# Kernel tuning notes

Measured on AMD Instinct MI355X. Metric: run time of the kernel, lower is better.

The kernel has to match this reference:

```python
import jax, jax.numpy as jnp
import numpy as np

# dims matching init_kwargs
B, C, T = 64, 8, 2048
K, DIL = 16, 4            # kernel_size, dilation
MLP = 16                  # mlp_dim
NF = min(MLP, K // 2 + 1) # n_frequencies = 9
FEAT = C * NF * 2         # 144
H1, H2 = 64, 32           # ReLUBlock hidden dims (64 -> 64//2)
EFF = DIL * (K - 1)       # 60
W = T - EFF               # 1988 windows


def setup_inputs() -> dict:
    key = jax.random.key(0)
    ks = jax.random.split(key, 10)
    def lin(k, out_d, in_d):
        kw, kb = jax.random.split(k)
        bound = 1.0 / np.sqrt(in_d)
        w = jax.random.uniform(kw, (out_d, in_d), jnp.float32, -bound, bound)
        b = jax.random.uniform(kb, (out_d,), jnp.float32, -bound, bound)
        return w, b
    x = jax.random.normal(ks[0], (B, C, T), jnp.float32)
    proj_w, proj_b = lin(ks[1], MLP, FEAT)
    w1, b1 = lin(ks[2], H1, MLP)
    w2, b2 = lin(ks[3], H2, H1)
    out_w, out_b = lin(ks[4], 1, H2)
    agg_w = jax.random.normal(ks[5], (W,), jnp.float32) * 0.1
    return {"x": x, "proj_w": proj_w, "proj_b": proj_b, "w1": w1, "b1": b1,
            "w2": w2, "b2": b2, "out_w": out_w, "out_b": out_b, "agg_w": agg_w}


def reference(x, proj_w, proj_b, w1, b1, w2, b2, out_w, out_b, agg_w):
    # Build all dilated windows at once: window[t, j] = x[..., t - (K-1-j)*DIL]
    starts = jnp.arange(EFF, T)                      # [W]
    offs = -(K - 1 - jnp.arange(K)) * DIL            # [K]
    idx = starts[:, None] + offs[None, :]            # [W, K]
    win = x[:, :, idx]                               # [B, C, W, K]
    f = jnp.fft.rfft(win, axis=-1)[..., :NF]         # [B, C, W, NF]
    mag = jnp.log1p(jnp.abs(f))
    ph = jnp.angle(f) / jnp.pi
    feat = jnp.stack([mag, ph], axis=-1)             # [B, C, W, NF, 2]
    feat = feat.transpose(0, 2, 1, 3, 4).reshape(B, W, FEAT)  # [B, W, C*NF*2]
    p = jnp.tanh(feat @ proj_w.T + proj_b) * jnp.pi  # [B, W, MLP]
    h = jax.nn.relu(p @ w1.T + b1)                   # [B, W, H1]
    h = jax.nn.relu(h @ w2.T + b2)                   # [B, W, H2]
    out = (h @ out_w.T + out_b)[..., 0]              # [B, W]
    wts = jax.nn.softmax(agg_w)                      # [W]
    return (out * wts[None, :]).sum(axis=1)          # [B]
```

## Files before the change

### kernel.cpp

```cpp
#include <hip/hip_runtime.h>
#include <math.h>

#define B_    64
#define C_    8
#define T_    2048
#define K_    16
#define NF_   9
#define FEAT_ 144
#define MLP_  16
#define H1_   64
#define H2_   32
#define EFF_  60
#define W_    1988
#define NWCH_ 8
#define NG_   4
#define PI_F  3.14159265358979323846f

constexpr float COS16[16] = {
   1.0f,  0.92387953251128674f,  0.70710678118654752f,  0.38268343236508977f,
   0.0f, -0.38268343236508977f, -0.70710678118654752f, -0.92387953251128674f,
  -1.0f, -0.92387953251128674f, -0.70710678118654752f, -0.38268343236508977f,
   0.0f,  0.38268343236508977f,  0.70710678118654752f,  0.92387953251128674f };
constexpr float SIN16F[16] = {
   0.0f,  0.38268343236508977f,  0.70710678118654752f,  0.92387953251128674f,
   1.0f,  0.92387953251128674f,  0.70710678118654752f,  0.38268343236508977f,
   0.0f, -0.38268343236508977f, -0.70710678118654752f, -0.92387953251128674f,
  -1.0f, -0.92387953251128674f, -0.70710678118654752f, -0.38268343236508977f };

__device__ __forceinline__ float fast_log1p(float s) {
  return __builtin_amdgcn_logf(1.0f + s) * 0.69314718055994531f;
}

__device__ __forceinline__ float atanpi_poly(float r) {
  const float s2 = r * r;
  float p = -0.0037310f;
  p = fmaf(p, s2,  0.0167600f);
  p = fmaf(p, s2, -0.0370617f);
  p = fmaf(p, s2,  0.0616068f);
  p = fmaf(p, s2, -0.10587734f);
  p = fmaf(p, s2,  0.31830265f);
  return r * p;
}

__device__ __forceinline__ float atan2pi_fast(float im, float re) {
  const float ax = fabsf(re), ay = fabsf(im);
  const float mx = fmaxf(ax, ay), mn = fminf(ax, ay);
  const float r = mn * __builtin_amdgcn_rcpf(fmaxf(mx, 1e-37f));
  float t = atanpi_poly(r);
  t = (ay > ax) ? 0.5f - t : t;
  t = (__float_as_uint(re) & 0x80000000u) ? 1.0f - t : t;
  return copysignf(t, im);
}

__device__ __forceinline__ float fast_tanh(float z) {
  const float az = fabsf(z);
  const float e = __builtin_amdgcn_exp2f(-2.8853900817779268f * az);
  const float th = fmaf(-2.0f, e * __builtin_amdgcn_rcpf(1.0f + e), 1.0f);
  return copysignf(th, z);
}

__device__ __forceinline__ void dft_proj_channel(const float* __restrict__ xc,
                                                 const float* __restrict__ PWt,
                                                 int c, float* pacc) {
  float win[K_];
  #pragma unroll
  for (int k = 0; k < K_; k++) win[k] = xc[k * 4];
  float ae[8], bo[8];
  #pragma unroll
  for (int k = 0; k < 8; k++) { ae[k] = win[k] + win[k+8]; bo[k] = win[k] - win[k+8]; }
  #pragma unroll
  for (int n = 0; n < NF_; n++) {
    float re = 0.f, im = 0.f;
    #pragma unroll
    for (int k = 0; k < 8; k++) {
      const float v = (n & 1) ? bo[k] : ae[k];
      const int t = (n * k) & 15;
      re = fmaf(v,  COS16[t],  re);
      im = fmaf(v, -SIN16F[t], im);
    }
    const float s   = __builtin_amdgcn_sqrtf(fmaf(re, re, im * im));
    const float mag = fast_log1p(s);
    const float ph  = atan2pi_fast(im, re);
    const float* rm = PWt + (size_t)((c * NF_ + n) * 2) * MLP_;
    #pragma unroll
    for (int j = 0; j < MLP_; j++)
      pacc[j] = fmaf(mag, rm[j], fmaf(ph, rm[MLP_ + j], pacc[j]));
  }
}

__device__ __forceinline__ float mlp_tail(const float* p,
                                          const float* __restrict__ w1, const float* __restrict__ b1,
                                          const float* __restrict__ W2t, const float* __restrict__ b2,
                                          const float* __restrict__ out_w, const float* __restrict__ out_b) {
  float h2a[H2_];
  #pragma unroll
  for (int m = 0; m < H2_; m++) h2a[m] = b2[m];
  #pragma unroll 8
  for (int i = 0; i < H1_; i++) {
    const float* r1 = w1 + i * MLP_;
    float acc = b1[i];
    #pragma unroll
    for (int j = 0; j < MLP_; j++) acc = fmaf(p[j], r1[j], acc);
    const float h1v = fmaxf(acc, 0.f);
    const float* r2 = W2t + i * H2_;
    #pragma unroll
    for (int m = 0; m < H2_; m++) h2a[m] = fmaf(h1v, r2[m], h2a[m]);
  }
  float o = out_b[0];
  #pragma unroll
  for (int m = 0; m < H2_; m++) o = fmaf(fmaxf(h2a[m], 0.f), out_w[m], o);
  return o;
}

__global__ __launch_bounds__(256) void setup_kernel(const float* __restrict__ agg,
                                                    float* __restrict__ wts,
                                                    const float* __restrict__ pw,
                                                    const float* __restrict__ w2,
                                                    float* __restrict__ PWt,
                                                    float* __restrict__ W2t) {
  if (blockIdx.x == 0) {
    __shared__ float red[256];
    const int tid = threadIdx.x;
    float m = -INFINITY;
    for (int i = tid; i < W_; i += 256) m = fmaxf(m, agg[i]);
    red[tid] = m; __syncthreads();
    for (int s = 128; s > 0; s >>= 1) { if (tid < s) red[tid] = fmaxf(red[tid], red[tid+s]); __syncthreads(); }
    const float mx = red[0];
    __syncthreads();
    float sum = 0.f;
    for (int i = tid; i < W_; i += 256) sum += expf(agg[i] - mx);
    red[tid] = sum; __syncthreads();
    for (int s = 128; s > 0; s >>= 1) { if (tid < s) red[tid] += red[tid+s]; __syncthreads(); }
    const float inv = 1.f / red[0];
    for (int i = tid; i < W_; i += 256) wts[i] = expf(agg[i] - mx) * inv;
  } else {
    const int tid = (blockIdx.x - 1) * 256 + threadIdx.x;
    if (tid < MLP_ * FEAT_) {
      const int j = tid / FEAT_, f = tid - j * FEAT_;
      PWt[f * MLP_ + j] = pw[tid];
    }
    if (tid < H2_ * H1_) {
      const int m = tid >> 6, i = tid & 63;
      W2t[i * H2_ + m] = w2[tid];
    }
  }
}

__global__ __launch_bounds__(256) void tcn_stage1(const float* __restrict__ x,
                                                  const float* __restrict__ PWt,
                                                  float* __restrict__ pf) {
  const int tid = threadIdx.x;
  const int b = blockIdx.y, g = blockIdx.z;
  const int w = blockIdx.x * 256 + tid;
  if (w >= W_) return;
  float pacc[MLP_];
  #pragma unroll
  for (int j = 0; j < MLP_; j++) pacc[j] = 0.f;
  #pragma unroll 1
  for (int cc = 0; cc < 2; cc++) {
    const int c = g * 2 + cc;
    dft_proj_channel(x + ((size_t)b * C_ + c) * T_ + w, PWt, c, pacc);
  }
  float4* dst = reinterpret_cast<float4*>(pf + ((size_t)(b * NG_ + g) * W_ + w) * MLP_);
  #pragma unroll
  for (int q = 0; q < 4; q++)
    dst[q] = make_float4(pacc[4*q+0], pacc[4*q+1], pacc[4*q+2], pacc[4*q+3]);
}

__global__ __launch_bounds__(256) void tcn_stage2(const float* __restrict__ pf,
                                                  const float* __restrict__ proj_b,
                                                  const float* __restrict__ w1, const float* __restrict__ b1,
                                                  const float* __restrict__ W2t, const float* __restrict__ b2,
                                                  const float* __restrict__ out_w, const float* __restrict__ out_b,
                                                  const float* __restrict__ wts, float* __restrict__ partials) {
  __shared__ float red[256];
  const int tid = threadIdx.x;
  const int b = blockIdx.y;
  const int w = blockIdx.x * 256 + tid;
  float val = 0.f;
  if (w < W_) {
    float pacc[MLP_];
    #pragma unroll
    for (int j = 0; j < MLP_; j++) pacc[j] = proj_b[j];
    #pragma unroll
    for (int g = 0; g < NG_; g++) {
      const float4* src = reinterpret_cast<const float4*>(pf + ((size_t)(b * NG_ + g) * W_ + w) * MLP_);
      #pragma unroll
      for (int q = 0; q < 4; q++) {
        const float4 a = src[q];
        pacc[4*q+0] += a.x; pacc[4*q+1] += a.y; pacc[4*q+2] += a.z; pacc[4*q+3] += a.w;
      }
    }
    float p[MLP_];
    #pragma unroll
    for (int j = 0; j < MLP_; j++) p[j] = fast_tanh(pacc[j]) * PI_F;
    val = mlp_tail(p, w1, b1, W2t, b2, out_w, out_b) * wts[w];
  }
  red[tid] = val; __syncthreads();
  for (int s = 128; s > 0; s >>= 1) { if (tid < s) red[tid] += red[tid+s]; __syncthreads(); }
  if (tid == 0) partials[b * NWCH_ + blockIdx.x] = red[0];
}

__global__ __launch_bounds__(256) void tcn_mono(const float* __restrict__ x,
                                                const float* __restrict__ PWt, const float* __restrict__ proj_b,
                                                const float* __restrict__ w1, const float* __restrict__ b1,
                                                const float* __restrict__ W2t, const float* __restrict__ b2,
                                                const float* __restrict__ out_w, const float* __restrict__ out_b,
                                                const float* __restrict__ wts, float* __restrict__ partials) {
  __shared__ float red[256];
  const int tid = threadIdx.x;
  const int b = blockIdx.y;
  const int w = blockIdx.x * 256 + tid;
  float val = 0.f;
  if (w < W_) {
    float pacc[MLP_];
    #pragma unroll
    for (int j = 0; j < MLP_; j++) pacc[j] = proj_b[j];
    #pragma unroll 1
    for (int c = 0; c < C_; c++)
      dft_proj_channel(x + ((size_t)b * C_ + c) * T_ + w, PWt, c, pacc);
    float p[MLP_];
    #pragma unroll
    for (int j = 0; j < MLP_; j++) p[j] = fast_tanh(pacc[j]) * PI_F;
    val = mlp_tail(p, w1, b1, W2t, b2, out_w, out_b) * wts[w];
  }
  red[tid] = val; __syncthreads();
  for (int s = 128; s > 0; s >>= 1) { if (tid < s) red[tid] += red[tid+s]; __syncthreads(); }
  if (tid == 0) partials[b * NWCH_ + blockIdx.x] = red[0];
}

__global__ void finalize_kernel(const float* __restrict__ partials, float* __restrict__ out) {
  const int b = threadIdx.x;
  if (b < B_) {
    float s = 0.f;
    #pragma unroll
    for (int c = 0; c < NWCH_; c++) s += partials[b * NWCH_ + c];
    out[b] = s;
  }
}

extern "C" void kernel_launch(void* const* d_in, const int* in_sizes, int n_in,
                              void* d_out, int out_size, void* d_ws, size_t ws_size,
                              hipStream_t stream) {
  const float* x      = (const float*)d_in[0];
  const float* proj_w = (const float*)d_in[1];
  const float* proj_b = (const float*)d_in[2];
  const float* w1     = (const float*)d_in[3];
  const float* b1     = (const float*)d_in[4];
  const float* w2     = (const float*)d_in[5];
  const float* b2     = (const float*)d_in[6];
  const float* out_w  = (const float*)d_in[7];
  const float* out_b  = (const float*)d_in[8];
  const float* agg_w  = (const float*)d_in[9];

  float* wts      = (float*)d_ws;
  float* partials = (float*)d_ws + 2048;
  float* PWt      = (float*)d_ws + 4096;
  float* W2t      = (float*)d_ws + 4096 + 2304;
  float* pf       = (float*)d_ws + 16384;

  const size_t need = ((size_t)16384 + (size_t)B_ * NG_ * W_ * MLP_) * sizeof(float);

  setup_kernel<<<10, 256, 0, stream>>>(agg_w, wts, proj_w, w2, PWt, W2t);
  if (ws_size >= need) {
    tcn_stage1<<<dim3(NWCH_, B_, NG_), 256, 0, stream>>>(x, PWt, pf);
    tcn_stage2<<<dim3(NWCH_, B_), 256, 0, stream>>>(pf, proj_b, w1, b1, W2t, b2,
                                                    out_w, out_b, wts, partials);
  } else {
    tcn_mono<<<dim3(NWCH_, B_), 256, 0, stream>>>(x, PWt, proj_b, w1, b1, W2t, b2,
                                                  out_w, out_b, wts, partials);
  }
  finalize_kernel<<<1, 64, 0, stream>>>(partials, (float*)d_out);
}
```

Before: 64.85 us.

## Split stage-2 MLP hidden units across four lanes per window with LDS weights

Stage 2 now gives each window to four lanes, each computing a quarter of the 64 hidden units. The W1 and W2 weights are staged in padded shared memory, and partial H2 sums are combined with cross-lane shuffles. The intermediate buffer is re-laid out so each 4-float group of a window sits contiguous across windows, which makes the loads coalesced. This raises stage-2 parallelism to 32 chunks per batch and cuts per-thread serial MLP work, at the cost of four redundant loads of the pf values per window and a shuffle reduction.

```diff
diff --git a/kernel.cpp b/kernel.cpp
--- a/kernel.cpp
+++ b/kernel.cpp
@@ -13,8 +13,11 @@
 #define EFF_  60
 #define W_    1988
 #define NWCH_ 8
+#define NCHK2 32
 #define NG_   4
 #define PI_F  3.14159265358979323846f
+#define STR1  20
+#define STR2  36
 
 constexpr float COS16[16] = {
    1.0f,  0.92387953251128674f,  0.70710678118654752f,  0.38268343236508977f,
@@ -161,44 +164,100 @@
     const int c = g * 2 + cc;
     dft_proj_channel(x + ((size_t)b * C_ + c) * T_ + w, PWt, c, pacc);
   }
-  float4* dst = reinterpret_cast<float4*>(pf + ((size_t)(b * NG_ + g) * W_ + w) * MLP_);
   #pragma unroll
   for (int q = 0; q < 4; q++)
-    dst[q] = make_float4(pacc[4*q+0], pacc[4*q+1], pacc[4*q+2], pacc[4*q+3]);
-}
-
-__global__ __launch_bounds__(256) void tcn_stage2(const float* __restrict__ pf,
-                                                  const float* __restrict__ proj_b,
-                                                  const float* __restrict__ w1, const float* __restrict__ b1,
-                                                  const float* __restrict__ W2t, const float* __restrict__ b2,
-                                                  const float* __restrict__ out_w, const float* __restrict__ out_b,
-                                                  const float* __restrict__ wts, float* __restrict__ partials) {
+    *reinterpret_cast<float4*>(pf + ((size_t)((b * NG_ + g) * 4 + q) * W_ + w) * 4) =
+        make_float4(pacc[4*q+0], pacc[4*q+1], pacc[4*q+2], pacc[4*q+3]);
+}
+
+__global__ __launch_bounds__(256) void tcn_stage2(
+    const float* __restrict__ pf, const float* __restrict__ proj_b,
+    const float* __restrict__ w1, const float* __restrict__ b1,
+    const float* __restrict__ W2t, const float* __restrict__ b2,
+    const float* __restrict__ out_w, const float* __restrict__ out_b,
+    const float* __restrict__ wts, float* __restrict__ partials) {
+  __shared__ __align__(16) float W1p[H1_ * STR1];
+  __shared__ __align__(16) float W2p[H1_ * STR2];
+  __shared__ float B1s[H1_];
   __shared__ float red[256];
   const int tid = threadIdx.x;
+  for (int idx = tid; idx < H1_ * MLP_; idx += 256) {
+    const int i = idx >> 4, j = idx & 15;
+    W1p[i * STR1 + j] = w1[idx];
+  }
+  for (int idx = tid; idx < H1_ * H2_; idx += 256) {
+    const int i = idx >> 5, m = idx & 31;
+    W2p[i * STR2 + m] = W2t[idx];
+  }
+  if (tid < H1_) B1s[tid] = b1[tid];
+  __syncthreads();
+
+  const int lane = tid & 63;
+  const int wave = tid >> 6;
+  const int wloc = lane & 15;
+  const int sub  = lane >> 4;
   const int b = blockIdx.y;
-  const int w = blockIdx.x * 256 + tid;
+  const int w = blockIdx.x * 64 + wave * 16 + wloc;
+  const int wl = (w < W_) ? w : 0;
+
+  float pacc[MLP_];
+  #pragma unroll
+  for (int j = 0; j < MLP_; j++) pacc[j] = proj_b[j];
+  #pragma unroll
+  for (int g = 0; g < NG_; g++) {
+    #pragma unroll
+    for (int q = 0; q < 4; q++) {
+      const float4 a = *reinterpret_cast<const float4*>(
+          pf + ((size_t)((b * NG_ + g) * 4 + q) * W_ + wl) * 4);
+      pacc[4*q+0] += a.x; pacc[4*q+1] += a.y; pacc[4*q+2] += a.z; pacc[4*q+3] += a.w;
+    }
+  }
+  float p[MLP_];
+  #pragma unroll
+  for (int j = 0; j < MLP_; j++) p[j] = fast_tanh(pacc[j]) * PI_F;
+
+  float h2a[H2_];
+  #pragma unroll
+  for (int m = 0; m < H2_; m++) h2a[m] = 0.f;
+  #pragma unroll 4
+  for (int ii = 0; ii < 16; ii++) {
+    const int i = sub + ii * 4;
+    const float4* r1 = reinterpret_cast<const float4*>(&W1p[i * STR1]);
+    float acc = B1s[i];
+    #pragma unroll
+    for (int q = 0; q < 4; q++) {
+      const float4 a = r1[q];
+      acc = fmaf(p[4*q+0], a.x, acc);
+      acc = fmaf(p[4*q+1], a.y, acc);
+      acc = fmaf(p[4*q+2], a.z, acc);
+      acc = fmaf(p[4*q+3], a.w, acc);
+    }
+    const float h1v = fmaxf(acc, 0.f);
+    const float4* r2 = reinterpret_cast<const float4*>(&W2p[i * STR2]);
+    #pragma unroll
+    for (int q = 0; q < 8; q++) {
+      const float4 a = r2[q];
+      h2a[4*q+0] = fmaf(h1v, a.x, h2a[4*q+0]);
+      h2a[4*q+1] = fmaf(h1v, a.y, h2a[4*q+1]);
+      h2a[4*q+2] = fmaf(h1v, a.z, h2a[4*q+2]);
+      h2a[4*q+3] = fmaf(h1v, a.w, h2a[4*q+3]);
+    }
+  }
+  #pragma unroll
+  for (int m = 0; m < H2_; m++) h2a[m] += __shfl_xor(h2a[m], 16, 64);
+  #pragma unroll
+  for (int m = 0; m < H2_; m++) h2a[m] += __shfl_xor(h2a[m], 32, 64);
+
   float val = 0.f;
-  if (w < W_) {
-    float pacc[MLP_];
-    #pragma unroll
-    for (int j = 0; j < MLP_; j++) pacc[j] = proj_b[j];
-    #pragma unroll
-    for (int g = 0; g < NG_; g++) {
-      const float4* src = reinterpret_cast<const float4*>(pf + ((size_t)(b * NG_ + g) * W_ + w) * MLP_);
-      #pragma unroll
-      for (int q = 0; q < 4; q++) {
-        const float4 a = src[q];
-        pacc[4*q+0] += a.x; pacc[4*q+1] += a.y; pacc[4*q+2] += a.z; pacc[4*q+3] += a.w;
-      }
-    }
-    float p[MLP_];
-    #pragma unroll
-    for (int j = 0; j < MLP_; j++) p[j] = fast_tanh(pacc[j]) * PI_F;
-    val = mlp_tail(p, w1, b1, W2t, b2, out_w, out_b) * wts[w];
+  if (sub == 0 && w < W_) {
+    float o = out_b[0];
+    #pragma unroll
+    for (int m = 0; m < H2_; m++) o = fmaf(fmaxf(h2a[m] + b2[m], 0.f), out_w[m], o);
+    val = o * wts[w];
   }
   red[tid] = val; __syncthreads();
   for (int s = 128; s > 0; s >>= 1) { if (tid < s) red[tid] += red[tid+s]; __syncthreads(); }
-  if (tid == 0) partials[b * NWCH_ + blockIdx.x] = red[0];
+  if (tid == 0) partials[b * NCHK2 + blockIdx.x] = red[0];
 }
 
 __global__ __launch_bounds__(256) void tcn_mono(const float* __restrict__ x,
@@ -229,12 +288,11 @@
   if (tid == 0) partials[b * NWCH_ + blockIdx.x] = red[0];
 }
 
-__global__ void finalize_kernel(const float* __restrict__ partials, float* __restrict__ out) {
+__global__ void finalize_kernel(const float* __restrict__ partials, float* __restrict__ out, int nchk) {
   const int b = threadIdx.x;
   if (b < B_) {
     float s = 0.f;
-    #pragma unroll
-    for (int c = 0; c < NWCH_; c++) s += partials[b * NWCH_ + c];
+    for (int c = 0; c < nchk; c++) s += partials[b * nchk + c];
     out[b] = s;
   }
 }
@@ -264,11 +322,12 @@
   setup_kernel<<<10, 256, 0, stream>>>(agg_w, wts, proj_w, w2, PWt, W2t);
   if (ws_size >= need) {
     tcn_stage1<<<dim3(NWCH_, B_, NG_), 256, 0, stream>>>(x, PWt, pf);
-    tcn_stage2<<<dim3(NWCH_, B_), 256, 0, stream>>>(pf, proj_b, w1, b1, W2t, b2,
+    tcn_stage2<<<dim3(NCHK2, B_), 256, 0, stream>>>(pf, proj_b, w1, b1, W2t, b2,
                                                     out_w, out_b, wts, partials);
+    finalize_kernel<<<1, 64, 0, stream>>>(partials, (float*)d_out, NCHK2);
   } else {
     tcn_mono<<<dim3(NWCH_, B_), 256, 0, stream>>>(x, PWt, proj_b, w1, b1, W2t, b2,
                                                   out_w, out_b, wts, partials);
-  }
-  finalize_kernel<<<1, 64, 0, stream>>>(partials, (float*)d_out);
-}
+    finalize_kernel<<<1, 64, 0, stream>>>(partials, (float*)d_out, NWCH_);
+  }
+}
```

Result: slower. 68.53 us (+5.7%).
